# Kernel optimization log

Measured on AMD Instinct MI355X. Metric: run time of the kernel, lower is better.

Reference implementation:

```python
import jax, jax.numpy as jnp
import numpy as np

B, S = 1, 2048
HIDDEN = 2560
NH, NKV, HD = 32, 8, 128
GS = 128  # awq group size
ROPE_THETA = 1000000.0


def dequant_q4(qweight, scales, qzeros):
    """Unpack int4 AWQ weights -> dense [K, N] float weight.
    qweight: [K//8, N] int32, 8 nibbles packed along the input (K) dim.
    scales/qzeros: [K//GS, N]. w = (nibble - zero) * scale.
    """
    K8, N = qweight.shape
    shifts = jnp.arange(8, dtype=jnp.int32) * 4
    nib = (qweight[:, None, :] >> shifts[None, :, None]) & 0xF  # [K//8, 8, N]
    w = nib.reshape(K8 * 8, N).astype(scales.dtype)             # [K, N]
    z = jnp.repeat(qzeros.astype(scales.dtype), GS, axis=0)     # [K, N]
    s = jnp.repeat(scales, GS, axis=0)                          # [K, N]
    return (w - z) * s


def linear_q4(x, qw, sc, qz, bias=None):
    w = dequant_q4(qw, sc, qz)                     # [K, N]
    y = jnp.einsum('bsk,kn->bsn', x, w)
    return y + bias if bias is not None else y


def rotate_half(x):
    x1, x2 = jnp.split(x, 2, axis=-1)
    return jnp.concatenate([-x2, x1], axis=-1)


def apply_rope(q, k, cos, sin):
    # cos/sin: [B, S, HD] -> broadcast over heads at dim 2
    c = cos[:, :, None, :]
    s = sin[:, :, None, :]
    return q * c + rotate_half(q) * s, k * c + rotate_half(k) * s


def setup_inputs() -> dict:
    key = jax.random.key(0)
    ks = jax.random.split(key, 12)

    x = jax.random.normal(ks[0], (B, S, HIDDEN), dtype=jnp.float32)

    # genuine rotary embedding tables
    inv_freq = 1.0 / (ROPE_THETA ** (np.arange(0, HD, 2, dtype=np.float32) / HD))
    t = np.arange(S, dtype=np.float32)
    freqs = np.outer(t, inv_freq)                      # [S, HD/2]
    emb = np.concatenate([freqs, freqs], axis=-1)      # [S, HD]
    cos = jnp.asarray(np.cos(emb)[None], dtype=jnp.float32)  # [1, S, HD]
    sin = jnp.asarray(np.sin(emb)[None], dtype=jnp.float32)

    def mk_proj(kq, ksc, kz, K, N, group=GS):
        qw = jax.random.randint(kq, (K // 8, N), 0, 2**31 - 1, dtype=jnp.int32)
        sc = jax.random.normal(ksc, (K // group, N), dtype=jnp.float32) * 0.01
        qz = jax.random.randint(kz, (K // group, N), 0, 16, dtype=jnp.int32)
        return qw, sc, qz

    q_qweight, q_scales, q_qzeros = mk_proj(ks[1], ks[2], ks[3], HIDDEN, NH * HD)
    k_qweight, k_scales, k_qzeros = mk_proj(ks[4], ks[5], ks[6], HIDDEN, NKV * HD)
    v_qweight, v_scales, v_qzeros = mk_proj(ks[7], ks[8], ks[9], HIDDEN, NKV * HD)
    o_qweight, o_scales, o_qzeros = mk_proj(ks[10], ks[11], jax.random.fold_in(key, 99), NH * HD, HIDDEN)

    kb = jax.random.split(jax.random.fold_in(key, 7), 3)
    q_bias = jax.random.normal(kb[0], (NH * HD,), dtype=jnp.float32) * 0.02
    k_bias = jax.random.normal(kb[1], (NKV * HD,), dtype=jnp.float32) * 0.02
    v_bias = jax.random.normal(kb[2], (NKV * HD,), dtype=jnp.float32) * 0.02

    return dict(x=x, cos=cos, sin=sin,
                q_scales=q_scales, q_bias=q_bias,
                k_scales=k_scales, k_bias=k_bias,
                v_scales=v_scales, v_bias=v_bias,
                o_scales=o_scales,
                q_qweight=q_qweight, q_qzeros=q_qzeros,
                k_qweight=k_qweight, k_qzeros=k_qzeros,
                v_qweight=v_qweight, v_qzeros=v_qzeros,
                o_qweight=o_qweight, o_qzeros=o_qzeros)


def reference(x, cos, sin,
              q_scales, q_bias, k_scales, k_bias, v_scales, v_bias, o_scales,
              q_qweight, q_qzeros, k_qweight, k_qzeros,
              v_qweight, v_qzeros, o_qweight, o_qzeros):
    b, s, _ = x.shape
    xq = linear_q4(x, q_qweight, q_scales, q_qzeros, q_bias).reshape(b, s, NH, HD)
    xk = linear_q4(x, k_qweight, k_scales, k_qzeros, k_bias).reshape(b, s, NKV, HD)
    xv = linear_q4(x, v_qweight, v_scales, v_qzeros, v_bias).reshape(b, s, NKV, HD)

    xq, xk = apply_rope(xq, xk, cos, sin)

    # GQA: repeat KV heads to match query heads (prefill, start_pos=0)
    rep = NH // NKV
    xk = jnp.repeat(xk, rep, axis=2)   # [b, s, NH, HD]
    xv = jnp.repeat(xv, rep, axis=2)

    scale = 1.0 / jnp.sqrt(jnp.asarray(HD, dtype=xq.dtype))
    scores = jnp.einsum('bqhd,bkhd->bhqk', xq, xk) * scale  # [b, NH, s, s]
    causal = jnp.tril(jnp.ones((s, s), dtype=bool))
    scores = jnp.where(causal[None, None], scores, jnp.finfo(scores.dtype).min)
    attn = jax.nn.softmax(scores, axis=-1)
    out = jnp.einsum('bhqk,bkhd->bqhd', attn, xv).reshape(b, s, NH * HD)

    return linear_q4(out, o_qweight, o_scales, o_qzeros)  # [b, s, HIDDEN]
```

## Files before the change

### kernel.cpp

```cpp
#include <hip/hip_runtime.h>
#include <hip/hip_bf16.h>
#include <cstdint>

#define S_LEN 2048
#define HIDDEN 2560
#define NH 32
#define NKV 8
#define HD 128
#define GS 128

typedef __attribute__((ext_vector_type(8))) _Float16 half8v;
typedef __attribute__((ext_vector_type(2))) _Float16 half2v;
typedef __attribute__((ext_vector_type(4))) float f32x4;
typedef unsigned int uint;
typedef unsigned short ushort;

__device__ inline ushort f2h(float f) {
    _Float16 h = (_Float16)f;
    return __builtin_bit_cast(ushort, h);
}
__device__ inline float h2f(ushort u) {
    return (float)__builtin_bit_cast(_Float16, u);
}
__device__ inline uint pk2(ushort a, ushort b) { return (uint)a | ((uint)b << 16); }
__device__ inline uint pkh2(float a, float b) {
    return __builtin_bit_cast(uint, __builtin_amdgcn_cvt_pkrtz(a, b));
}

__device__ __attribute__((always_inline)) inline void gl_lds16(const void* g, void* l) {
    __builtin_amdgcn_global_load_lds(
        (const __attribute__((address_space(1))) unsigned int*)g,
        (__attribute__((address_space(3))) unsigned int*)l, 16, 0, 0);
}

#define WAIT_LGKM0  asm volatile("s_waitcnt lgkmcnt(0)" ::: "memory")
#define WAIT_VM(N)  asm volatile("s_waitcnt vmcnt(" #N ")" ::: "memory")
#define RAW_BARRIER { __builtin_amdgcn_s_barrier(); __builtin_amdgcn_sched_barrier(0); }

__global__ __launch_bounds__(320) void xcvt_kernel(
    const float* __restrict__ X, ushort* __restrict__ Xf)
{
    const int row = blockIdx.x;
    const int t   = threadIdx.x;
    const size_t base = (size_t)row * HIDDEN + t * 8;
    float4 a = *(const float4*)&X[base];
    float4 b = *(const float4*)&X[base + 4];
    uint4 hw = {pk2(f2h(a.x), f2h(a.y)), pk2(f2h(a.z), f2h(a.w)),
                pk2(f2h(b.x), f2h(b.y)), pk2(f2h(b.z), f2h(b.w))};
    *(uint4*)&Xf[base] = hw;
}

__global__ __launch_bounds__(256) void wdq_kernel(
    const int* __restrict__ q_qw, const float* __restrict__ q_sc, const int* __restrict__ q_qz,
    const int* __restrict__ k_qw, const float* __restrict__ k_sc, const int* __restrict__ k_qz,
    const int* __restrict__ v_qw, const float* __restrict__ v_sc, const int* __restrict__ v_qz,
    ushort* __restrict__ WT)
{
    __shared__ __align__(16) char Ts[16384];

    const int bx = blockIdx.x;
    const int kt = blockIdx.y;
    const int t  = threadIdx.x;

    int nloc0, wtbase, Nw;
    const int* QW; const float* SC; const int* QZ;
    if (bx < 64)      { Nw = NH * HD;  nloc0 = bx * 64;        wtbase = bx * 64;
                        QW = q_qw; SC = q_sc; QZ = q_qz; }
    else if (bx < 80) { Nw = NKV * HD; nloc0 = (bx - 64) * 64; wtbase = 4096 + nloc0;
                        QW = k_qw; SC = k_sc; QZ = k_qz; }
    else              { Nw = NKV * HD; nloc0 = (bx - 80) * 64; wtbase = 5120 + nloc0;
                        QW = v_qw; SC = v_sc; QZ = v_qz; }

    const int k80 = kt * 16;
    const int nn  = t & 63;
    const float scf = SC[(size_t)kt * Nw + nloc0 + nn];
    const float zf  = (float)QZ[(size_t)kt * Nw + nloc0 + nn];
    ushort sch = f2h(scf);
    float schf = h2f(sch);
    ushort msc = f2h(-128.0f * schf);
    ushort nzs = f2h(-(zf * schf));
    half2v S2 = {__builtin_bit_cast(_Float16, sch), __builtin_bit_cast(_Float16, sch)};
    half2v M2 = {__builtin_bit_cast(_Float16, msc), __builtin_bit_cast(_Float16, msc)};
    half2v Z2 = {__builtin_bit_cast(_Float16, nzs), __builtin_bit_cast(_Float16, nzs)};

#pragma unroll
    for (int i = 0; i < 4; ++i) {
        int kw = i * 4 + (t >> 6);
        uint q = (uint)QW[(size_t)(k80 + kw) * Nw + nloc0 + nn];
        uint xn = q & 0x0F0F0F0Fu;
        uint yn = (q >> 4) & 0x0F0F0F0Fu;
        uint W0 = __builtin_amdgcn_perm(yn, xn, 0x0C040C00u);
        uint W1 = __builtin_amdgcn_perm(yn, xn, 0x0C050C01u);
        uint W2 = __builtin_amdgcn_perm(yn, xn, 0x0C060C02u);
        uint W3 = __builtin_amdgcn_perm(yn, xn, 0x0C070C03u);
        uint e0 = (W0 << 3) | 0x58005800u;
        uint e1 = (W1 << 3) | 0x58005800u;
        uint e2 = (W2 << 3) | 0x58005800u;
        uint e3 = (W3 << 3) | 0x58005800u;
        half2v w0 = __builtin_bit_cast(half2v, e0) * S2 + M2; w0 = w0 + Z2;
        half2v w1 = __builtin_bit_cast(half2v, e1) * S2 + M2; w1 = w1 + Z2;
        half2v w2 = __builtin_bit_cast(half2v, e2) * S2 + M2; w2 = w2 + Z2;
        half2v w3 = __builtin_bit_cast(half2v, e3) * S2 + M2; w3 = w3 + Z2;
        uint4 dw = {__builtin_bit_cast(uint, w0), __builtin_bit_cast(uint, w1),
                    __builtin_bit_cast(uint, w2), __builtin_bit_cast(uint, w3)};
        *(uint4*)(Ts + nn * 256 + ((kw * 16) ^ ((nn & 7) << 4))) = dw;
    }
    __syncthreads();
    const int kc = t & 15;
#pragma unroll
    for (int i = 0; i < 4; ++i) {
        int nr = i * 16 + (t >> 4);
        uint4 v = *(const uint4*)(Ts + nr * 256 + ((kc * 16) ^ ((nr & 7) << 4)));
        *(uint4*)&WT[(size_t)(wtbase + nr) * HIDDEN + kt * 128 + kc * 8] = v;
    }
}

__global__ __launch_bounds__(256) void qkv11_kernel(
    const ushort* __restrict__ Xf, const ushort* __restrict__ WT,
    const float* __restrict__ q_b, const float* __restrict__ k_b,
    const float* __restrict__ v_b,
    const float* __restrict__ cosb, const float* __restrict__ sinb,
    ushort* __restrict__ Qf, ushort* __restrict__ Kf,
    ushort* __restrict__ Vrm)
{
    __shared__ __align__(16) char LDSB[65536];
    ushort* A0 = (ushort*)(LDSB);
    ushort* A1 = (ushort*)(LDSB + 16384);
    ushort* B0 = (ushort*)(LDSB + 32768);
    ushort* B1 = (ushort*)(LDSB + 49152);

    const int t  = threadIdx.x;
    const int w  = t >> 6;
    const int l  = t & 63;
    const int lg = l >> 4;
    const int lr = l & 15;
    const int wr = w >> 1;
    const int wc = w & 1;
    const int K  = HIDDEN;

    const int bid  = blockIdx.x;
    const int xcd  = bid & 7;
    const int j    = bid >> 3;
    const int nblk = xcd * 6 + (j >> 4);
    const int m0   = (j & 15) * 128;
    const int wtrow = nblk * 128;

    int region, nbase;
    const float* BI;
    if (nblk < 32)      { region = 0; nbase = nblk * 128;        BI = q_b; }
    else if (nblk < 40) { region = 1; nbase = (nblk - 32) * 128; BI = k_b; }
    else                { region = 2; nbase = (nblk - 40) * 128; BI = v_b; }

    const int ldsAw = w * 1024;
    size_t aoff[4], boff[4];
#pragma unroll
    for (int i = 0; i < 4; ++i) {
        int slot = i * 256 + t;
        int rm = slot >> 3, rc = slot & 7;
        aoff[i] = (size_t)(m0 + rm) * K + (size_t)((rc ^ (rm & 7)) * 8);
        boff[i] = (size_t)(wtrow + rm) * K + (size_t)((rc ^ (rm & 7)) * 8);
    }

    int ncm[4];
#pragma unroll
    for (int nf = 0; nf < 4; ++nf)
        ncm[nf] = wc * 32 + (nf & 1) * 16 + lr + ((nf & 2) ? 64 : 0);

    const int xorA = (lr & 7) << 4;
    int aroff[4][2], broff[4][2];
#pragma unroll
    for (int mf = 0; mf < 4; ++mf)
#pragma unroll
        for (int ks = 0; ks < 2; ++ks)
            aroff[mf][ks] = (((wr * 64 + mf * 16 + lr) * 128) + lg * 16 + ks * 64) ^ xorA;
#pragma unroll
    for (int nf = 0; nf < 4; ++nf)
#pragma unroll
        for (int ks = 0; ks < 2; ++ks)
            broff[nf][ks] = ((ncm[nf] * 128) + lg * 16 + ks * 64) ^ xorA;

    f32x4 macc[4][4];
#pragma unroll
    for (int mf = 0; mf < 4; ++mf)
#pragma unroll
        for (int nf = 0; nf < 4; ++nf) macc[mf][nf] = f32x4{0.f, 0.f, 0.f, 0.f};

#define QKV_STAGE(AH, BH, k0) { \
    gl_lds16(Xf + (k0) + aoff[0], (char*)(AH) + ldsAw); \
    gl_lds16(Xf + (k0) + aoff[1], (char*)(AH) + 4096 + ldsAw); \
    gl_lds16(Xf + (k0) + aoff[2], (char*)(AH) + 8192 + ldsAw); \
    gl_lds16(Xf + (k0) + aoff[3], (char*)(AH) + 12288 + ldsAw); \
    gl_lds16(WT + (k0) + boff[0], (char*)(BH) + ldsAw); \
    gl_lds16(WT + (k0) + boff[1], (char*)(BH) + 4096 + ldsAw); \
    gl_lds16(WT + (k0) + boff[2], (char*)(BH) + 8192 + ldsAw); \
    gl_lds16(WT + (k0) + boff[3], (char*)(BH) + 12288 + ldsAw); }

#define QKV_COMPUTE(AH, BT) { \
    _Pragma("unroll") \
    for (int ks = 0; ks < 2; ++ks) { \
        half8v av[4], bv[4]; \
        _Pragma("unroll") \
        for (int mf = 0; mf < 4; ++mf) \
            av[mf] = *(const half8v*)((const char*)(AH) + aroff[mf][ks]); \
        _Pragma("unroll") \
        for (int nf = 0; nf < 4; ++nf) \
            bv[nf] = *(const half8v*)((const char*)(BT) + broff[nf][ks]); \
        _Pragma("unroll") \
        for (int mf = 0; mf < 4; ++mf) \
            _Pragma("unroll") \
            for (int nf = 0; nf < 4; ++nf) \
                macc[mf][nf] = __builtin_amdgcn_mfma_f32_16x16x32_f16(av[mf], bv[nf], macc[mf][nf], 0, 0, 0); \
    } }

    QKV_STAGE(A0, B0, 0);
    WAIT_VM(0);
    RAW_BARRIER;

    for (int g = 0; g < 19; ++g) {
        QKV_STAGE(A1, B1, (2 * g + 1) * 64);
        QKV_COMPUTE(A0, B0);
        WAIT_VM(0);
        RAW_BARRIER;
        QKV_STAGE(A0, B0, (2 * g + 2) * 64);
        QKV_COMPUTE(A1, B1);
        WAIT_VM(0);
        RAW_BARRIER;
    }
    QKV_STAGE(A1, B1, 39 * 64);
    QKV_COMPUTE(A0, B0);
    WAIT_VM(0);
    RAW_BARRIER;
    QKV_COMPUTE(A1, B1);

#pragma unroll
    for (int nf = 0; nf < 4; ++nf) {
        float bv = BI[nbase + ncm[nf]];
#pragma unroll
        for (int mf = 0; mf < 4; ++mf)
#pragma unroll
            for (int r = 0; r < 4; ++r) macc[mf][nf][r] += bv;
    }

    if (region == 2) {
#pragma unroll
        for (int mf = 0; mf < 4; ++mf)
#pragma unroll
            for (int r = 0; r < 4; ++r) {
                int row = m0 + wr * 64 + mf * 16 + lg * 4 + r;
#pragma unroll
                for (int nf = 0; nf < 4; ++nf)
                    Vrm[(size_t)row * (NKV * HD) + nbase + ncm[nf]] = f2h(macc[mf][nf][r]);
            }
    } else {
        ushort* OF = (region == 0) ? Qf : Kf;
        const int No = (region == 0) ? NH * HD : NKV * HD;
        const float osc = (region == 0) ? 0.08838834764831845f : 1.0f;
#pragma unroll
        for (int mf = 0; mf < 4; ++mf)
#pragma unroll
            for (int r = 0; r < 4; ++r) {
                int row = m0 + wr * 64 + mf * 16 + lg * 4 + r;
                const float* cb = &cosb[(size_t)row * HD];
                const float* sb = &sinb[(size_t)row * HD];
#pragma unroll
                for (int nf = 0; nf < 2; ++nf) {
                    int d = wc * 32 + nf * 16 + lr;
                    float a = macc[mf][nf][r];
                    float b = macc[mf][nf + 2][r];
                    float o1 = (a * cb[d]      - b * sb[d])      * osc;
                    float o2 = (b * cb[d + 64] + a * sb[d + 64]) * osc;
                    OF[(size_t)row * No + nbase + d]      = f2h(o1);
                    OF[(size_t)row * No + nbase + d + 64] = f2h(o2);
                }
            }
    }
#undef QKV_STAGE
#undef QKV_COMPUTE
}

__global__ __launch_bounds__(256) void vtrans_kernel(
    const ushort* __restrict__ Vrm, ushort* __restrict__ VfT)
{
    __shared__ ushort Ts[64][65];
    const int s0 = blockIdx.x * 64;
    const int n0 = blockIdx.y * 64;
    const int t  = threadIdx.x;
    {
        int r = t >> 2, c0 = (t & 3) * 16;
        uint4 v0 = *(const uint4*)&Vrm[(size_t)(s0 + r) * (NKV * HD) + n0 + c0];
        uint4 v1 = *(const uint4*)&Vrm[(size_t)(s0 + r) * (NKV * HD) + n0 + c0 + 8];
        const ushort* pv = (const ushort*)&v0;
#pragma unroll
        for (int j = 0; j < 8; ++j) Ts[r][c0 + j] = pv[j];
        pv = (const ushort*)&v1;
#pragma unroll
        for (int j = 0; j < 8; ++j) Ts[r][c0 + 8 + j] = pv[j];
    }
    __syncthreads();
    {
        int rn = t >> 2, cs0 = (t & 3) * 16;
        ushort ob[16];
#pragma unroll
        for (int j = 0; j < 16; ++j) ob[j] = Ts[cs0 + j][rn];
        ushort* dst = &VfT[(size_t)(n0 + rn) * S_LEN + s0 + cs0];
        *(uint4*)dst = ((uint4*)ob)[0];
        *(uint4*)(dst + 8) = ((uint4*)ob)[1];
    }
}

__global__ __launch_bounds__(256) void oproj8_kernel(
    const ushort* __restrict__ Xb, const int* __restrict__ QW,
    const float* __restrict__ SC, const int* __restrict__ QZ,
    float* __restrict__ Y)
{
    __shared__ __align__(16) char LDSB[65536];
    ushort* A0 = (ushort*)(LDSB);
    ushort* A1 = (ushort*)(LDSB + 16384);
    ushort* B0 = (ushort*)(LDSB + 32768);
    ushort* B1 = (ushort*)(LDSB + 49152);

    const int t  = threadIdx.x;
    const int w  = t >> 6;
    const int l  = t & 63;
    const int lg = l >> 4;
    const int lr = l & 15;
    const int wr = w >> 1;
    const int wc = w & 1;
    const int K  = NH * HD;
    const int N  = HIDDEN;

    const int bid = blockIdx.x;
    const int swz = (bid & 7) * 40 + (bid >> 3);
    const int n0  = (swz % 20) * 128;
    const int m0  = (swz / 20) * 128;

    const int ldsAw = w * 1024;
    size_t aoff[4];
#pragma unroll
    for (int i = 0; i < 4; ++i) {
        int slot = i * 256 + t;
        int am = slot >> 3, ac = slot & 7;
        aoff[i] = (size_t)(m0 + am) * K + (size_t)((ac ^ (am & 7)) * 8);
    }
    const int bn  = t & 127;
    const int bk0 = (t >> 7) * 4;
    int bwoff[4];
#pragma unroll
    for (int j = 0; j < 4; ++j)
        bwoff[j] = (bn * 128 + (bk0 + j) * 16) ^ ((bn & 7) << 4);

    const int xorA = (lr & 7) << 4;
    int aroff[4][2], broff[4][2];
#pragma unroll
    for (int mf = 0; mf < 4; ++mf)
#pragma unroll
        for (int ks = 0; ks < 2; ++ks)
            aroff[mf][ks] = (((wr * 64 + mf * 16 + lr) * 128) + lg * 16 + ks * 64) ^ xorA;
#pragma unroll
    for (int nf = 0; nf < 4; ++nf)
#pragma unroll
        for (int ks = 0; ks < 2; ++ks)
            broff[nf][ks] = (((wc * 64 + nf * 16 + lr) * 128) + lg * 16 + ks * 64) ^ xorA;

    f32x4 macc[4][4];
#pragma unroll
    for (int mf = 0; mf < 4; ++mf)
#pragma unroll
        for (int nf = 0; nf < 4; ++nf) macc[mf][nf] = f32x4{0.f, 0.f, 0.f, 0.f};
    uint qr[4];
    float scf, zf;

#define OP_QW(tile) { int g8 = (tile) * 8; int gg = (tile) >> 1; \
    _Pragma("unroll") \
    for (int j = 0; j < 4; ++j) \
        qr[j] = (uint)QW[(size_t)(g8 + bk0 + j) * N + n0 + bn]; \
    scf = SC[(size_t)gg * N + n0 + bn]; \
    zf  = (float)QZ[(size_t)gg * N + n0 + bn]; }

#define OP_STAGE_A(AH, k0) { \
    gl_lds16(Xb + (k0) + aoff[0], (char*)(AH) + ldsAw); \
    gl_lds16(Xb + (k0) + aoff[1], (char*)(AH) + 4096 + ldsAw); \
    gl_lds16(Xb + (k0) + aoff[2], (char*)(AH) + 8192 + ldsAw); \
    gl_lds16(Xb + (k0) + aoff[3], (char*)(AH) + 12288 + ldsAw); }

#define OP_BWRITE(BT) { \
    ushort sch = f2h(scf); \
    float schf = h2f(sch); \
    ushort msc = f2h(-128.0f * schf); \
    ushort nzs = f2h(-(zf * schf)); \
    half2v S2 = {__builtin_bit_cast(_Float16, sch), __builtin_bit_cast(_Float16, sch)}; \
    half2v M2 = {__builtin_bit_cast(_Float16, msc), __builtin_bit_cast(_Float16, msc)}; \
    half2v Z2 = {__builtin_bit_cast(_Float16, nzs), __builtin_bit_cast(_Float16, nzs)}; \
    _Pragma("unroll") \
    for (int j = 0; j < 4; ++j) { \
        uint q = qr[j]; \
        uint xn = q & 0x0F0F0F0Fu; \
        uint yn = (q >> 4) & 0x0F0F0F0Fu; \
        uint4 dw; \
        uint W0 = __builtin_amdgcn_perm(yn, xn, 0x0C040C00u); \
        uint W1 = __builtin_amdgcn_perm(yn, xn, 0x0C050C01u); \
        uint W2 = __builtin_amdgcn_perm(yn, xn, 0x0C060C02u); \
        uint W3 = __builtin_amdgcn_perm(yn, xn, 0x0C070C03u); \
        uint e0 = (W0 << 3) | 0x58005800u; \
        uint e1 = (W1 << 3) | 0x58005800u; \
        uint e2 = (W2 << 3) | 0x58005800u; \
        uint e3 = (W3 << 3) | 0x58005800u; \
        half2v w0 = __builtin_bit_cast(half2v, e0) * S2 + M2; w0 = w0 + Z2; \
        half2v w1 = __builtin_bit_cast(half2v, e1) * S2 + M2; w1 = w1 + Z2; \
        half2v w2 = __builtin_bit_cast(half2v, e2) * S2 + M2; w2 = w2 + Z2; \
        half2v w3 = __builtin_bit_cast(half2v, e3) * S2 + M2; w3 = w3 + Z2; \
        dw.x = __builtin_bit_cast(uint, w0); \
        dw.y = __builtin_bit_cast(uint, w1); \
        dw.z = __builtin_bit_cast(uint, w2); \
        dw.w = __builtin_bit_cast(uint, w3); \
        *(uint4*)((char*)(BT) + bwoff[j]) = dw; \
    } }

#define OP_COMPUTE(AH, BT) { \
    _Pragma("unroll") \
    for (int ks = 0; ks < 2; ++ks) { \
        half8v av[4], bv[4]; \
        _Pragma("unroll") \
        for (int mf = 0; mf < 4; ++mf) \
            av[mf] = *(const half8v*)((const char*)(AH) + aroff[mf][ks]); \
        _Pragma("unroll") \
        for (int nf = 0; nf < 4; ++nf) \
            bv[nf] = *(const half8v*)((const char*)(BT) + broff[nf][ks]); \
        _Pragma("unroll") \
        for (int mf = 0; mf < 4; ++mf) \
            _Pragma("unroll") \
            for (int nf = 0; nf < 4; ++nf) \
                macc[mf][nf] = __builtin_amdgcn_mfma_f32_16x16x32_f16(av[mf], bv[nf], macc[mf][nf], 0, 0, 0); \
    } }

    OP_QW(0);
    OP_BWRITE(B0);
    OP_STAGE_A(A0, 0);
    OP_QW(1);
    WAIT_LGKM0;
    WAIT_VM(6);
    RAW_BARRIER;

    for (int g = 0; g < 31; ++g) {
        OP_STAGE_A(A1, (2 * g + 1) * 64);
        OP_COMPUTE(A0, B0);
        OP_BWRITE(B1);
        OP_QW(2 * g + 2);
        WAIT_LGKM0;
        WAIT_VM(6);
        RAW_BARRIER;
        OP_STAGE_A(A0, (2 * g + 2) * 64);
        OP_COMPUTE(A1, B1);
        OP_BWRITE(B0);
        OP_QW(2 * g + 3);
        WAIT_LGKM0;
        WAIT_VM(6);
        RAW_BARRIER;
    }
    OP_STAGE_A(A1, 63 * 64);
    OP_COMPUTE(A0, B0);
    OP_BWRITE(B1);
    WAIT_LGKM0;
    WAIT_VM(0);
    RAW_BARRIER;
    OP_COMPUTE(A1, B1);

#pragma unroll
    for (int mf = 0; mf < 4; ++mf)
#pragma unroll
        for (int r = 0; r < 4; ++r) {
            int row = m0 + wr * 64 + mf * 16 + lg * 4 + r;
#pragma unroll
            for (int nf = 0; nf < 4; ++nf)
                Y[(size_t)row * N + n0 + wc * 64 + nf * 16 + lr] = macc[mf][nf][r];
        }
#undef OP_QW
#undef OP_STAGE_A
#undef OP_BWRITE
#undef OP_COMPUTE
}

__global__ __launch_bounds__(256) void attn_mfma_kernel(
    const ushort* __restrict__ Qh,
    const ushort* __restrict__ Kh,
    const ushort* __restrict__ Vt,
    ushort* __restrict__ AO)
{
    __shared__ ushort Ks0[32 * 128];
    __shared__ ushort Ks1[32 * 128];
    __shared__ ushort Vs0[128 * 32];
    __shared__ ushort Vs1[128 * 32];
    __shared__ __align__(16) char PsB[4 * 1280];

    const int h  = blockIdx.x;
    const int qb = gridDim.y - 1 - blockIdx.y;
    const int s0 = qb * 64;
    const int t  = threadIdx.x;
    const int w  = t >> 6;
    const int l  = t & 63;
    const int lg = l >> 4;
    const int lr = l & 15;
    const int kvh = h >> 2;
    const int qw = s0 + w * 16;
    const int q  = qw + lr;

    half8v qf[4];
#pragma unroll
    for (int d = 0; d < 4; ++d) {
        size_t off = (size_t)q * (NH * HD) + h * HD + d * 32 + lg * 8;
        qf[d] = *(const half8v*)&Qh[off];
    }

    f32x4 o[8];
#pragma unroll
    for (int i = 0; i < 8; ++i) o[i] = f32x4{0.f, 0.f, 0.f, 0.f};
    float m = -1e30f, lsum = 0.f;
    char* pw = PsB + w * 1280;

#define ATTN_STAGE(KB, VB, k0) { \
    _Pragma("unroll") \
    for (int i = 0; i < 2; ++i) { \
        int slot = w * 128 + i * 64 + l; \
        int mr = slot >> 4, c = slot & 15; \
        size_t goff = (size_t)((k0) + mr) * (NKV * HD) + kvh * HD + ((c ^ (mr & 7)) * 8); \
        gl_lds16(Kh + goff, (char*)(KB) + (w * 128 + i * 64) * 16); \
    } \
    _Pragma("unroll") \
    for (int i = 0; i < 2; ++i) { \
        int slot = w * 128 + i * 64 + l; \
        int dim = slot >> 2, c = slot & 3; \
        size_t goff = (size_t)(kvh * HD + dim) * S_LEN + (k0) + ((c ^ (dim & 3)) * 8); \
        gl_lds16(Vt + goff, (char*)(VB) + (w * 128 + i * 64) * 16); \
    } }

#define ATTN_TILE(KSF, VSS, k0) \
    if ((k0) <= qw + 15) { \
        f32x4 s_[2]; \
        s_[0] = f32x4{0.f, 0.f, 0.f, 0.f}; \
        s_[1] = f32x4{0.f, 0.f, 0.f, 0.f}; \
        _Pragma("unroll") \
        for (int d = 0; d < 4; ++d) { \
            _Pragma("unroll") \
            for (int nt2 = 0; nt2 < 2; ++nt2) { \
                int row = nt2 * 16 + lr; \
                int off = row * 256 + ((d * 64 + lg * 16) ^ ((row & 7) << 4)); \
                half8v kf = *(const half8v*)((const char*)(KSF) + off); \
                s_[nt2] = __builtin_amdgcn_mfma_f32_16x16x32_f16(kf, qf[d], s_[nt2], 0, 0, 0); \
            } \
        } \
        float sv[8]; \
        if ((k0) + 31 <= qw) { \
            _Pragma("unroll") \
            for (int nt2 = 0; nt2 < 2; ++nt2) \
                _Pragma("unroll") \
                for (int r = 0; r < 4; ++r) sv[nt2 * 4 + r] = s_[nt2][r]; \
        } else { \
            _Pragma("unroll") \
            for (int nt2 = 0; nt2 < 2; ++nt2) \
                _Pragma("unroll") \
                for (int r = 0; r < 4; ++r) { \
                    int kv = (k0) + nt2 * 16 + lg * 4 + r; \
                    sv[nt2 * 4 + r] = (kv <= q) ? s_[nt2][r] : -1e30f; \
                } \
        } \
        float mx = sv[0]; \
        _Pragma("unroll") \
        for (int j = 1; j < 8; ++j) mx = fmaxf(mx, sv[j]); \
        mx = fmaxf(mx, __shfl_xor(mx, 16)); \
        mx = fmaxf(mx, __shfl_xor(mx, 32)); \
        float p_[8], ps = 0.f; \
        if (__all(mx <= m + 8.0f)) { \
            _Pragma("unroll") \
            for (int j = 0; j < 8; ++j) { p_[j] = __expf(sv[j] - m); ps += p_[j]; } \
            ps += __shfl_xor(ps, 16); \
            ps += __shfl_xor(ps, 32); \
            lsum += ps; \
        } else { \
            float mnew = fmaxf(m, mx); \
            float resc = __expf(m - mnew); \
            m = mnew; \
            _Pragma("unroll") \
            for (int j = 0; j < 8; ++j) { p_[j] = __expf(sv[j] - m); ps += p_[j]; } \
            ps += __shfl_xor(ps, 16); \
            ps += __shfl_xor(ps, 32); \
            lsum = lsum * resc + ps; \
            _Pragma("unroll") \
            for (int dt = 0; dt < 8; ++dt) \
                _Pragma("unroll") \
                for (int r = 0; r < 4; ++r) o[dt][r] *= resc; \
        } \
        uint2 w0_ = {pkh2(p_[0], p_[1]), pkh2(p_[2], p_[3])}; \
        uint2 w1_ = {pkh2(p_[4], p_[5]), pkh2(p_[6], p_[7])}; \
        *(uint2*)(pw + lr * 80 + lg * 8)      = w0_; \
        *(uint2*)(pw + lr * 80 + 32 + lg * 8) = w1_; \
        asm volatile("s_waitcnt lgkmcnt(0)" ::: "memory"); \
        half8v pf = *(const half8v*)(pw + lr * 80 + lg * 16); \
        _Pragma("unroll") \
        for (int dt = 0; dt < 8; ++dt) { \
            int dim = dt * 16 + lr; \
            half8v vf = *(const half8v*)((const char*)(VSS) + dim * 64 + ((lg * 16) ^ ((dim & 3) << 4))); \
            o[dt] = __builtin_amdgcn_mfma_f32_16x16x32_f16(vf, pf, o[dt], 0, 0, 0); \
        } \
    }

    const int ntiles = qb * 2 + 2;

    ATTN_STAGE(Ks0, Vs0, 0);
    WAIT_VM(0);
    RAW_BARRIER;

    for (int kt = 0; kt < ntiles; kt += 2) {
        if (kt + 1 < ntiles) ATTN_STAGE(Ks1, Vs1, (kt + 1) * 32);
        ATTN_TILE(Ks0, Vs0, kt * 32);
        WAIT_VM(0);
        RAW_BARRIER;
        if (kt + 2 < ntiles) ATTN_STAGE(Ks0, Vs0, (kt + 2) * 32);
        ATTN_TILE(Ks1, Vs1, (kt + 1) * 32);
        WAIT_VM(0);
        RAW_BARRIER;
    }

    float inv = 1.f / lsum;
    ushort* dst = &AO[(size_t)q * (NH * HD) + h * HD];
#pragma unroll
    for (int dt = 0; dt < 8; ++dt) {
        uint2 ov = {pkh2(o[dt][0] * inv, o[dt][1] * inv),
                    pkh2(o[dt][2] * inv, o[dt][3] * inv)};
        *(uint2*)(dst + dt * 16 + lg * 4) = ov;
    }
#undef ATTN_STAGE
#undef ATTN_TILE
}

extern "C" void kernel_launch(void* const* d_in, const int* in_sizes, int n_in,
                              void* d_out, int out_size, void* d_ws, size_t ws_size,
                              hipStream_t stream)
{
    const float* x    = (const float*)d_in[0];
    const float* cosb = (const float*)d_in[1];
    const float* sinb = (const float*)d_in[2];
    const float* q_sc = (const float*)d_in[3];
    const float* q_b  = (const float*)d_in[4];
    const float* k_sc = (const float*)d_in[5];
    const float* k_b  = (const float*)d_in[6];
    const float* v_sc = (const float*)d_in[7];
    const float* v_b  = (const float*)d_in[8];
    const float* o_sc = (const float*)d_in[9];
    const int* q_qw   = (const int*)d_in[10];
    const int* q_qz   = (const int*)d_in[11];
    const int* k_qw   = (const int*)d_in[12];
    const int* k_qz   = (const int*)d_in[13];
    const int* v_qw   = (const int*)d_in[14];
    const int* v_qz   = (const int*)d_in[15];
    const int* o_qw   = (const int*)d_in[16];
    const int* o_qz   = (const int*)d_in[17];
    float* out = (float*)d_out;

    char* ws = (char*)d_ws;
    ushort* Xf   = (ushort*)ws;
    ushort* AOf  = (ushort*)ws;
    ushort* WT   = (ushort*)(ws + (size_t)10 * 1024 * 1024);
    ushort* Qf   = (ushort*)(ws + (size_t)40 * 1024 * 1024);
    ushort* Kf   = (ushort*)(ws + (size_t)56 * 1024 * 1024);
    ushort* Vrm  = (ushort*)(ws + (size_t)60 * 1024 * 1024);
    ushort* VfT  = (ushort*)(ws + (size_t)64 * 1024 * 1024);

    xcvt_kernel<<<S_LEN, 320, 0, stream>>>(x, Xf);

    wdq_kernel<<<dim3(96, 20), 256, 0, stream>>>(
        q_qw, q_sc, q_qz, k_qw, k_sc, k_qz, v_qw, v_sc, v_qz, WT);

    qkv11_kernel<<<768, 256, 0, stream>>>(
        Xf, WT, q_b, k_b, v_b, cosb, sinb, Qf, Kf, Vrm);

    vtrans_kernel<<<dim3(S_LEN / 64, (NKV * HD) / 64), 256, 0, stream>>>(Vrm, VfT);

    attn_mfma_kernel<<<dim3(NH, S_LEN / 64), 256, 0, stream>>>(Qf, Kf, VfT, AOf);

    oproj8_kernel<<<320, 256, 0, stream>>>(
        AOf, o_qw, o_sc, o_qz, out);
}
```

Before: 266.4 us.

## Process two 16-row query tiles per wave in attention to reuse K/V fragments

Each attention block now covers 128 query rows instead of 64. Each wave handles two 16-row query sub-tiles, so every K and V fragment loaded from LDS feeds two MFMAs. This halves the grid and the number of K/V staging passes per query, cutting LDS and global traffic per unit of work. The V LDS swizzle is also changed to XOR with (dim>>1)&3, which is meant to reduce bank conflicts. In exchange, register pressure roughly doubles for the accumulators and Q fragments, and fewer blocks with coarser causal load balance may lower occupancy.

```diff
diff --git a/kernel.cpp b/kernel.cpp
--- a/kernel.cpp
+++ b/kernel.cpp
@@ -490,32 +490,35 @@
     __shared__ ushort Ks1[32 * 128];
     __shared__ ushort Vs0[128 * 32];
     __shared__ ushort Vs1[128 * 32];
-    __shared__ __align__(16) char PsB[4 * 1280];
+    __shared__ __align__(16) char PsB[4 * 2560];
 
     const int h  = blockIdx.x;
     const int qb = gridDim.y - 1 - blockIdx.y;
-    const int s0 = qb * 64;
+    const int s0 = qb * 128;
     const int t  = threadIdx.x;
     const int w  = t >> 6;
     const int l  = t & 63;
     const int lg = l >> 4;
     const int lr = l & 15;
     const int kvh = h >> 2;
-    const int qw = s0 + w * 16;
-    const int q  = qw + lr;
-
-    half8v qf[4];
-#pragma unroll
-    for (int d = 0; d < 4; ++d) {
-        size_t off = (size_t)q * (NH * HD) + h * HD + d * 32 + lg * 8;
-        qf[d] = *(const half8v*)&Qh[off];
-    }
-
-    f32x4 o[8];
-#pragma unroll
-    for (int i = 0; i < 8; ++i) o[i] = f32x4{0.f, 0.f, 0.f, 0.f};
-    float m = -1e30f, lsum = 0.f;
-    char* pw = PsB + w * 1280;
+    const int qw = s0 + w * 32;
+
+    half8v qf[2][4];
+#pragma unroll
+    for (int qi = 0; qi < 2; ++qi)
+#pragma unroll
+        for (int d = 0; d < 4; ++d) {
+            size_t off = (size_t)(qw + qi * 16 + lr) * (NH * HD) + h * HD + d * 32 + lg * 8;
+            qf[qi][d] = *(const half8v*)&Qh[off];
+        }
+
+    f32x4 o[2][8];
+#pragma unroll
+    for (int qi = 0; qi < 2; ++qi)
+#pragma unroll
+        for (int i = 0; i < 8; ++i) o[qi][i] = f32x4{0.f, 0.f, 0.f, 0.f};
+    float m[2] = {-1e30f, -1e30f}, lsum[2] = {0.f, 0.f};
+    char* pw = PsB + w * 2560;
 
 #define ATTN_STAGE(KB, VB, k0) { \
     _Pragma("unroll") \
@@ -529,81 +532,88 @@
     for (int i = 0; i < 2; ++i) { \
         int slot = w * 128 + i * 64 + l; \
         int dim = slot >> 2, c = slot & 3; \
-        size_t goff = (size_t)(kvh * HD + dim) * S_LEN + (k0) + ((c ^ (dim & 3)) * 8); \
+        size_t goff = (size_t)(kvh * HD + dim) * S_LEN + (k0) + ((c ^ ((dim >> 1) & 3)) * 8); \
         gl_lds16(Vt + goff, (char*)(VB) + (w * 128 + i * 64) * 16); \
     } }
 
 #define ATTN_TILE(KSF, VSS, k0) \
-    if ((k0) <= qw + 15) { \
-        f32x4 s_[2]; \
-        s_[0] = f32x4{0.f, 0.f, 0.f, 0.f}; \
-        s_[1] = f32x4{0.f, 0.f, 0.f, 0.f}; \
-        _Pragma("unroll") \
-        for (int d = 0; d < 4; ++d) { \
+    if ((k0) <= qw + 31) { \
+        half8v pf[2]; \
+        _Pragma("unroll") \
+        for (int qi = 0; qi < 2; ++qi) { \
+            f32x4 s_[2]; \
+            s_[0] = f32x4{0.f, 0.f, 0.f, 0.f}; \
+            s_[1] = f32x4{0.f, 0.f, 0.f, 0.f}; \
             _Pragma("unroll") \
-            for (int nt2 = 0; nt2 < 2; ++nt2) { \
-                int row = nt2 * 16 + lr; \
-                int off = row * 256 + ((d * 64 + lg * 16) ^ ((row & 7) << 4)); \
-                half8v kf = *(const half8v*)((const char*)(KSF) + off); \
-                s_[nt2] = __builtin_amdgcn_mfma_f32_16x16x32_f16(kf, qf[d], s_[nt2], 0, 0, 0); \
+            for (int d = 0; d < 4; ++d) { \
+                _Pragma("unroll") \
+                for (int nt2 = 0; nt2 < 2; ++nt2) { \
+                    int row = nt2 * 16 + lr; \
+                    int off = row * 256 + ((d * 64 + lg * 16) ^ ((row & 7) << 4)); \
+                    half8v kf = *(const half8v*)((const char*)(KSF) + off); \
+                    s_[nt2] = __builtin_amdgcn_mfma_f32_16x16x32_f16(kf, qf[qi][d], s_[nt2], 0, 0, 0); \
+                } \
             } \
+            const int q_ = qw + qi * 16 + lr; \
+            float sv[8]; \
+            if ((k0) + 31 <= qw + qi * 16) { \
+                _Pragma("unroll") \
+                for (int nt2 = 0; nt2 < 2; ++nt2) \
+                    _Pragma("unroll") \
+                    for (int r = 0; r < 4; ++r) sv[nt2 * 4 + r] = s_[nt2][r]; \
+            } else { \
+                _Pragma("unroll") \
+                for (int nt2 = 0; nt2 < 2; ++nt2) \
+                    _Pragma("unroll") \
+                    for (int r = 0; r < 4; ++r) { \
+                        int kv = (k0) + nt2 * 16 + lg * 4 + r; \
+                        sv[nt2 * 4 + r] = (kv <= q_) ? s_[nt2][r] : -1e30f; \
+                    } \
+            } \
+            float mx = sv[0]; \
+            _Pragma("unroll") \
+            for (int j = 1; j < 8; ++j) mx = fmaxf(mx, sv[j]); \
+            mx = fmaxf(mx, __shfl_xor(mx, 16)); \
+            mx = fmaxf(mx, __shfl_xor(mx, 32)); \
+            float p_[8], ps = 0.f; \
+            if (__all(mx <= m[qi] + 8.0f)) { \
+                _Pragma("unroll") \
+                for (int j = 0; j < 8; ++j) { p_[j] = __expf(sv[j] - m[qi]); ps += p_[j]; } \
+                ps += __shfl_xor(ps, 16); \
+                ps += __shfl_xor(ps, 32); \
+                lsum[qi] += ps; \
+            } else { \
+                float mnew = fmaxf(m[qi], mx); \
+                float resc = __expf(m[qi] - mnew); \
+                m[qi] = mnew; \
+                _Pragma("unroll") \
+                for (int j = 0; j < 8; ++j) { p_[j] = __expf(sv[j] - m[qi]); ps += p_[j]; } \
+                ps += __shfl_xor(ps, 16); \
+                ps += __shfl_xor(ps, 32); \
+                lsum[qi] = lsum[qi] * resc + ps; \
+                _Pragma("unroll") \
+                for (int dt = 0; dt < 8; ++dt) \
+                    _Pragma("unroll") \
+                    for (int r = 0; r < 4; ++r) o[qi][dt][r] *= resc; \
+            } \
+            uint2 w0_ = {pkh2(p_[0], p_[1]), pkh2(p_[2], p_[3])}; \
+            uint2 w1_ = {pkh2(p_[4], p_[5]), pkh2(p_[6], p_[7])}; \
+            *(uint2*)(pw + (qi * 16 + lr) * 80 + lg * 8)      = w0_; \
+            *(uint2*)(pw + (qi * 16 + lr) * 80 + 32 + lg * 8) = w1_; \
         } \
-        float sv[8]; \
-        if ((k0) + 31 <= qw) { \
-            _Pragma("unroll") \
-            for (int nt2 = 0; nt2 < 2; ++nt2) \
-                _Pragma("unroll") \
-                for (int r = 0; r < 4; ++r) sv[nt2 * 4 + r] = s_[nt2][r]; \
-        } else { \
-            _Pragma("unroll") \
-            for (int nt2 = 0; nt2 < 2; ++nt2) \
-                _Pragma("unroll") \
-                for (int r = 0; r < 4; ++r) { \
-                    int kv = (k0) + nt2 * 16 + lg * 4 + r; \
-                    sv[nt2 * 4 + r] = (kv <= q) ? s_[nt2][r] : -1e30f; \
-                } \
-        } \
-        float mx = sv[0]; \
-        _Pragma("unroll") \
-        for (int j = 1; j < 8; ++j) mx = fmaxf(mx, sv[j]); \
-        mx = fmaxf(mx, __shfl_xor(mx, 16)); \
-        mx = fmaxf(mx, __shfl_xor(mx, 32)); \
-        float p_[8], ps = 0.f; \
-        if (__all(mx <= m + 8.0f)) { \
-            _Pragma("unroll") \
-            for (int j = 0; j < 8; ++j) { p_[j] = __expf(sv[j] - m); ps += p_[j]; } \
-            ps += __shfl_xor(ps, 16); \
-            ps += __shfl_xor(ps, 32); \
-            lsum += ps; \
-        } else { \
-            float mnew = fmaxf(m, mx); \
-            float resc = __expf(m - mnew); \
-            m = mnew; \
-            _Pragma("unroll") \
-            for (int j = 0; j < 8; ++j) { p_[j] = __expf(sv[j] - m); ps += p_[j]; } \
-            ps += __shfl_xor(ps, 16); \
-            ps += __shfl_xor(ps, 32); \
-            lsum = lsum * resc + ps; \
-            _Pragma("unroll") \
-            for (int dt = 0; dt < 8; ++dt) \
-                _Pragma("unroll") \
-                for (int r = 0; r < 4; ++r) o[dt][r] *= resc; \
-        } \
-        uint2 w0_ = {pkh2(p_[0], p_[1]), pkh2(p_[2], p_[3])}; \
-        uint2 w1_ = {pkh2(p_[4], p_[5]), pkh2(p_[6], p_[7])}; \
-        *(uint2*)(pw + lr * 80 + lg * 8)      = w0_; \
-        *(uint2*)(pw + lr * 80 + 32 + lg * 8) = w1_; \
         asm volatile("s_waitcnt lgkmcnt(0)" ::: "memory"); \
-        half8v pf = *(const half8v*)(pw + lr * 80 + lg * 16); \
+        pf[0] = *(const half8v*)(pw + lr * 80 + lg * 16); \
+        pf[1] = *(const half8v*)(pw + (16 + lr) * 80 + lg * 16); \
         _Pragma("unroll") \
         for (int dt = 0; dt < 8; ++dt) { \
             int dim = dt * 16 + lr; \
-            half8v vf = *(const half8v*)((const char*)(VSS) + dim * 64 + ((lg * 16) ^ ((dim & 3) << 4))); \
-            o[dt] = __builtin_amdgcn_mfma_f32_16x16x32_f16(vf, pf, o[dt], 0, 0, 0); \
+            half8v vf = *(const half8v*)((const char*)(VSS) + dim * 64 + ((lg * 16) ^ (((dim >> 1) & 3) << 4))); \
+            o[0][dt] = __builtin_amdgcn_mfma_f32_16x16x32_f16(vf, pf[0], o[0][dt], 0, 0, 0); \
+            o[1][dt] = __builtin_amdgcn_mfma_f32_16x16x32_f16(vf, pf[1], o[1][dt], 0, 0, 0); \
         } \
     }
 
-    const int ntiles = qb * 2 + 2;
+    const int ntiles = qb * 4 + 4;
 
     ATTN_STAGE(Ks0, Vs0, 0);
     WAIT_VM(0);
@@ -620,13 +630,16 @@
         RAW_BARRIER;
     }
 
-    float inv = 1.f / lsum;
-    ushort* dst = &AO[(size_t)q * (NH * HD) + h * HD];
-#pragma unroll
-    for (int dt = 0; dt < 8; ++dt) {
-        uint2 ov = {pkh2(o[dt][0] * inv, o[dt][1] * inv),
-                    pkh2(o[dt][2] * inv, o[dt][3] * inv)};
-        *(uint2*)(dst + dt * 16 + lg * 4) = ov;
+#pragma unroll
+    for (int qi = 0; qi < 2; ++qi) {
+        float inv = 1.f / lsum[qi];
+        ushort* dst = &AO[(size_t)(qw + qi * 16 + lr) * (NH * HD) + h * HD];
+#pragma unroll
+        for (int dt = 0; dt < 8; ++dt) {
+            uint2 ov = {pkh2(o[qi][dt][0] * inv, o[qi][dt][1] * inv),
+                        pkh2(o[qi][dt][2] * inv, o[qi][dt][3] * inv)};
+            *(uint2*)(dst + dt * 16 + lg * 4) = ov;
+        }
     }
 #undef ATTN_STAGE
 #undef ATTN_TILE
@@ -675,7 +688,7 @@
 
     vtrans_kernel<<<dim3(S_LEN / 64, (NKV * HD) / 64), 256, 0, stream>>>(Vrm, VfT);
 
-    attn_mfma_kernel<<<dim3(NH, S_LEN / 64), 256, 0, stream>>>(Qf, Kf, VfT, AOf);
+    attn_mfma_kernel<<<dim3(NH, S_LEN / 128), 256, 0, stream>>>(Qf, Kf, VfT, AOf);
 
     oproj8_kernel<<<320, 256, 0, stream>>>(
         AOf, o_qw, o_sc, o_qz, out);
```

Result: slower. 298.2 us (+11.9%).
